# Performance work log

Hardware: AMD Instinct MI355X
Metric: run time of the kernel (lower is better)

Reference implementation:

```python
import jax, jax.numpy as jnp
import numpy as np

B, N, F_IN = 32, 512, 16
H, D_HID, D_OUT = 8, 8, 32
ALPHA = 0.2
NEG = -9e15


def setup_inputs() -> dict:
    key = jax.random.key(0)
    ks = jax.random.split(key, 10)
    xv = jax.random.normal(ks[0], (B, N, F_IN), dtype=jnp.float32)
    adj = (jax.random.uniform(ks[1], (B, N, N)) < 0.05).astype(jnp.float32)
    s = 0.1
    W_heads = jax.random.normal(ks[2], (H, F_IN, D_HID), dtype=jnp.float32) * s
    a1 = jax.random.normal(ks[3], (H, D_HID), dtype=jnp.float32) * s
    a2 = jax.random.normal(ks[4], (H, D_HID), dtype=jnp.float32) * s
    W_out = jax.random.normal(ks[5], (H * D_HID, D_OUT), dtype=jnp.float32) * s
    a1_out = jax.random.normal(ks[6], (D_OUT,), dtype=jnp.float32) * s
    a2_out = jax.random.normal(ks[7], (D_OUT,), dtype=jnp.float32) * s
    W_q = jax.random.normal(ks[8], (N * D_OUT, N), dtype=jnp.float32) * s
    b_q = jax.random.normal(ks[9], (N,), dtype=jnp.float32) * s
    return {"xv": xv, "adj": adj, "W_heads": W_heads, "a1": a1, "a2": a2,
            "W_out": W_out, "a1_out": a1_out, "a2_out": a2_out,
            "W_q": W_q, "b_q": b_q}


def _masked_softmax(e, adj_mask):
    # e: [..., N, N]; adj_mask broadcastable bool
    scores = jnp.where(adj_mask, e, NEG)
    return jax.nn.softmax(scores, axis=-1)


def reference(xv, adj, W_heads, a1, a2, W_out, a1_out, a2_out, W_q, b_q):
    mask = adj > 0  # [B, N, N]
    # --- multi-head GAT layer (vectorized over batch and heads) ---
    Wh = jnp.einsum('bnf,hfd->bhnd', xv, W_heads)            # [B,H,N,Dh]
    f1 = jnp.einsum('bhnd,hd->bhn', Wh, a1)                   # a^T[:Dh] . Wh_i
    f2 = jnp.einsum('bhnd,hd->bhn', Wh, a2)                   # a^T[Dh:] . Wh_j
    e = jax.nn.leaky_relu(f1[:, :, :, None] + f2[:, :, None, :], ALPHA)  # [B,H,N,N]
    att = _masked_softmax(e, mask[:, None, :, :])
    h = jnp.einsum('bhnm,bhmd->bhnd', att, Wh)
    h = jax.nn.elu(h)                                         # concat=True heads apply elu
    h_cat = jnp.transpose(h, (0, 2, 1, 3)).reshape(B, N, H * D_HID)  # head-major concat
    # --- output attention layer (concat=False: no internal elu) ---
    Who = jnp.einsum('bnf,fd->bnd', h_cat, W_out)             # [B,N,Do]
    g1 = Who @ a1_out                                         # [B,N]
    g2 = Who @ a2_out
    eo = jax.nn.leaky_relu(g1[:, :, None] + g2[:, None, :], ALPHA)
    att_o = _masked_softmax(eo, mask)
    out = jnp.einsum('bnm,bmd->bnd', att_o, Who)
    out = jax.nn.elu(out)                                     # F.elu applied in forward
    # --- Q head ---
    q = out.reshape(B, N * D_OUT) @ W_q + b_q                 # [B,N]
    return q[..., None]                                       # [B,N,1]
```

## Files before the change

### kernel.cpp

```cpp
#include <hip/hip_runtime.h>
#include <stdint.h>


typedef unsigned long long u64;

__device__ __forceinline__ float eluf(float x) { return x > 0.f ? x : __expf(x) - 1.f; }
__device__ __forceinline__ float lrelu(float x) { return fmaxf(x, 0.2f * x); }

__device__ u64   g_mask[131072];
__device__ float g_hcat[1048576];
__device__ float g_Who[524288];
__device__ float g_g1[16384];
__device__ float g_g2[16384];
__device__ float g_out2[524288];
__device__ float g_partial[4194304];

__global__ __launch_bounds__(256) void k_mask(const float* __restrict__ adj) {
  int wid = blockIdx.x * 4 + (threadIdx.x >> 6);
  int lane = threadIdx.x & 63;
#pragma unroll
  for (int seg = 0; seg < 16; ++seg) {
    int gw = wid * 16 + seg;
    float v = adj[(size_t)(gw >> 3) * 512 + (gw & 7) * 64 + lane];
    u64 bal = __ballot(v > 0.f);
    if (lane == 0) g_mask[gw] = bal;
  }
}

__global__ __launch_bounds__(512) void k_gat(const float* __restrict__ xv,
                                             const float* __restrict__ whd,
                                             const float* __restrict__ a1,
                                             const float* __restrict__ a2) {
  __shared__ float w_s[128];
  __shared__ float a1s[8], a2s[8];
  __shared__ float wh_lo[2048];
  __shared__ float wh_hi[2048];
  __shared__ float f2s[512];

  int bh = blockIdx.x;
  int b = bh >> 3, h = bh & 7;
  int tid = threadIdx.x;

  const u64* mrow = g_mask + (size_t)b * 4096 + (size_t)tid * 8;
  u64 mreg[8];
#pragma unroll
  for (int w = 0; w < 8; ++w) mreg[w] = mrow[w];

  if (tid < 128) w_s[tid] = whd[h * 128 + tid];
  if (tid < 8) { a1s[tid] = a1[h * 8 + tid]; a2s[tid] = a2[h * 8 + tid]; }
  __syncthreads();

  const float4* xp = (const float4*)(xv + (size_t)(b * 512 + tid) * 16);
  float x[16];
#pragma unroll
  for (int i = 0; i < 4; ++i) {
    float4 v = xp[i];
    x[4 * i] = v.x; x[4 * i + 1] = v.y; x[4 * i + 2] = v.z; x[4 * i + 3] = v.w;
  }
  float wh[8] = {0, 0, 0, 0, 0, 0, 0, 0};
#pragma unroll
  for (int f = 0; f < 16; ++f) {
    float xf = x[f];
#pragma unroll
    for (int d = 0; d < 8; ++d) wh[d] += xf * w_s[f * 8 + d];
  }
  float f1v = 0.f, s2 = 0.f;
#pragma unroll
  for (int d = 0; d < 8; ++d) { f1v += wh[d] * a1s[d]; s2 += wh[d] * a2s[d]; }
  f2s[tid] = s2;
  *(float4*)(wh_lo + tid * 4) = make_float4(wh[0], wh[1], wh[2], wh[3]);
  *(float4*)(wh_hi + tid * 4) = make_float4(wh[4], wh[5], wh[6], wh[7]);
  __syncthreads();

  float acc[8] = {0, 0, 0, 0, 0, 0, 0, 0};
  float sum = 0.f;
#pragma unroll
  for (int w = 0; w < 8; ++w) {
    u64 mq = mreg[w];
    while (mq) {
      int j = __builtin_ctzll(mq);
      mq &= mq - 1;
      int col = w * 64 + j;
      float p = __expf(lrelu(f1v + f2s[col]));
      sum += p;
      float4 A = *(const float4*)(wh_lo + col * 4);
      float4 Bv = *(const float4*)(wh_hi + col * 4);
      acc[0] += p * A.x;  acc[1] += p * A.y;  acc[2] += p * A.z;  acc[3] += p * A.w;
      acc[4] += p * Bv.x; acc[5] += p * Bv.y; acc[6] += p * Bv.z; acc[7] += p * Bv.w;
    }
  }

  float rs = sum > 0.f ? 1.0f / sum : 0.f;
  float* dst = g_hcat + (size_t)(b * 512 + tid) * 64 + h * 8;
  *(float4*)dst = make_float4(eluf(acc[0] * rs), eluf(acc[1] * rs), eluf(acc[2] * rs), eluf(acc[3] * rs));
  *(float4*)(dst + 4) = make_float4(eluf(acc[4] * rs), eluf(acc[5] * rs), eluf(acc[6] * rs), eluf(acc[7] * rs));
}

__global__ __launch_bounds__(128) void k_who(const float* __restrict__ wout,
                                             const float* __restrict__ a1o,
                                             const float* __restrict__ a2o) {
  __shared__ float wo_s[2048];
  __shared__ float a1s[32], a2s[32];
  int tid = threadIdx.x;
  for (int i = tid; i < 2048; i += 128) wo_s[i] = wout[i];
  if (tid < 32) { a1s[tid] = a1o[tid]; a2s[tid] = a2o[tid]; }
  __syncthreads();

  int idx = blockIdx.x * 128 + tid;
  int g = idx >> 1;
  int db = (idx & 1) * 16;

  const float4* hp = (const float4*)(g_hcat + (size_t)g * 64);
  float acc[16];
#pragma unroll
  for (int d = 0; d < 16; ++d) acc[d] = 0.f;
#pragma unroll
  for (int f4 = 0; f4 < 16; ++f4) {
    float4 h4 = hp[f4];
    float hv[4] = {h4.x, h4.y, h4.z, h4.w};
#pragma unroll
    for (int k = 0; k < 4; ++k) {
      const float* wr = wo_s + (f4 * 4 + k) * 32 + db;
      float hvk = hv[k];
#pragma unroll
      for (int d = 0; d < 16; ++d) acc[d] += hvk * wr[d];
    }
  }
  float s1 = 0.f, s2 = 0.f;
#pragma unroll
  for (int d = 0; d < 16; ++d) { s1 += acc[d] * a1s[db + d]; s2 += acc[d] * a2s[db + d]; }
  s1 += __shfl_xor(s1, 1);
  s2 += __shfl_xor(s2, 1);

  float* wdst = g_Who + (size_t)g * 32 + db;
#pragma unroll
  for (int d4 = 0; d4 < 4; ++d4)
    *(float4*)(wdst + d4 * 4) = make_float4(acc[d4 * 4], acc[d4 * 4 + 1], acc[d4 * 4 + 2], acc[d4 * 4 + 3]);
  if ((idx & 1) == 0) { g_g1[g] = s1; g_g2[g] = s2; }
}

__global__ __launch_bounds__(512) void k_att2() {
  __shared__ float pool[9216];
  __shared__ float g2c[256];
  __shared__ u64 mask_s[512];

  int b = blockIdx.x >> 3;
  int t = blockIdx.x & 7;
  int tid = threadIdx.x;
  int w = tid >> 6;
  int l = tid & 63;

  mask_s[tid] = g_mask[(size_t)b * 4096 + t * 512 + tid];
  float g1v = g_g1[(size_t)b * 512 + t * 64 + l];

  float acc[32];
#pragma unroll
  for (int d = 0; d < 32; ++d) acc[d] = 0.f;
  float sum = 0.f;

#pragma unroll 1
  for (int c = 0; c < 2; ++c) {
    __syncthreads();
    {
      const float4* src = (const float4*)g_Who + (size_t)b * 4096;
      for (int i = tid; i < 2048; i += 512) {
        int m = i >> 3, d4 = i & 7;
        *(float4*)(pool + m * 36 + d4 * 4) = src[c * 2048 + i];
      }
      if (tid < 64) ((float4*)g2c)[tid] = ((const float4*)g_g2)[(size_t)b * 128 + c * 64 + tid];
    }
    __syncthreads();
    u64 mq = mask_s[l * 8 + c * 4 + (w >> 1)];
    uint32_t bits = (w & 1) ? (uint32_t)(mq >> 32) : (uint32_t)mq;
    while (bits) {
      int j = __builtin_ctz(bits);
      bits &= bits - 1;
      float p = __expf(lrelu(g1v + g2c[w * 32 + j]));
      sum += p;
      const float* wq = pool + (w * 32 + j) * 36;
#pragma unroll
      for (int d4 = 0; d4 < 8; ++d4) {
        float4 v = *(const float4*)(wq + d4 * 4);
        acc[d4 * 4]     += p * v.x;
        acc[d4 * 4 + 1] += p * v.y;
        acc[d4 * 4 + 2] += p * v.z;
        acc[d4 * 4 + 3] += p * v.w;
      }
    }
  }

#pragma unroll 1
  for (int step = 4; step >= 1; step >>= 1) {
    __syncthreads();
    if (w >= step && w < 2 * step) {
      float* rp = pool + (size_t)((w - step) * 64 + l) * 36;
#pragma unroll
      for (int d4 = 0; d4 < 8; ++d4)
        *(float4*)(rp + d4 * 4) = make_float4(acc[d4 * 4], acc[d4 * 4 + 1], acc[d4 * 4 + 2], acc[d4 * 4 + 3]);
      rp[32] = sum;
    }
    __syncthreads();
    if (w < step) {
      const float* rp = pool + (size_t)(w * 64 + l) * 36;
#pragma unroll
      for (int d = 0; d < 32; ++d) acc[d] += rp[d];
      sum += rp[32];
    }
  }

  if (w == 0) {
    float rs = sum > 0.f ? 1.0f / sum : 0.f;
    float* dst = g_out2 + (size_t)(b * 512 + t * 64 + l) * 32;
#pragma unroll
    for (int d4 = 0; d4 < 8; ++d4)
      *(float4*)(dst + d4 * 4) = make_float4(eluf(acc[d4 * 4] * rs), eluf(acc[d4 * 4 + 1] * rs),
                                             eluf(acc[d4 * 4 + 2] * rs), eluf(acc[d4 * 4 + 3] * rs));
  }
}

__global__ __launch_bounds__(512) void k_qpart(const float* __restrict__ Wq) {
  __shared__ float outS[64 * 36];
  int s = blockIdx.x >> 1;
  int c = blockIdx.x & 1;
  int tid = threadIdx.x;
  int lane = tid & 63;
  int bg = tid >> 6;

  if (tid < 512) {
    int i = tid;
    int bb = i >> 4, kk4 = (i & 15) * 4;
    float4 v = *(const float4*)(g_out2 + (size_t)bb * 16384 + s * 64 + kk4);
    outS[(kk4 + 0) * 36 + bb] = v.x;
    outS[(kk4 + 1) * 36 + bb] = v.y;
    outS[(kk4 + 2) * 36 + bb] = v.z;
    outS[(kk4 + 3) * 36 + bb] = v.w;
  }
  __syncthreads();

  const float* wp = Wq + (size_t)(s * 64) * 512 + c * 256 + lane * 4;
  float4 acc[4];
#pragma unroll
  for (int j = 0; j < 4; ++j) acc[j] = make_float4(0.f, 0.f, 0.f, 0.f);

#pragma unroll 8
  for (int kk = 0; kk < 64; ++kk) {
    float4 wv = *(const float4*)(wp + (size_t)kk * 512);
    const float* ob = outS + kk * 36 + bg * 4;
    float4 o = *(const float4*)(ob);
    float ov[4] = {o.x, o.y, o.z, o.w};
#pragma unroll
    for (int j = 0; j < 4; ++j) {
      acc[j].x += ov[j] * wv.x; acc[j].y += ov[j] * wv.y;
      acc[j].z += ov[j] * wv.z; acc[j].w += ov[j] * wv.w;
    }
  }
#pragma unroll
  for (int j = 0; j < 4; ++j)
    *(float4*)(g_partial + (size_t)(s * 32 + bg * 4 + j) * 512 + c * 256 + lane * 4) = acc[j];
}

__global__ __launch_bounds__(256) void k_qred(const float* __restrict__ bq,
                                              float* __restrict__ out) {
  __shared__ float red[4][64];
  int tid = threadIdx.x;
  int w = tid >> 6, lane = tid & 63;
  int g = blockIdx.x * 64 + lane;
  int b = g >> 9, np = g & 511;

  float q = 0.f;
#pragma unroll 8
  for (int i = 0; i < 64; ++i) {
    int s = w + i * 4;
    q += g_partial[(size_t)(s * 32 + b) * 512 + np];
  }
  red[w][lane] = q;
  __syncthreads();
  if (w == 0)
    out[g] = bq[np] + red[0][lane] + red[1][lane] + red[2][lane] + red[3][lane];
}

extern "C" void kernel_launch(void* const* d_in, const int* in_sizes, int n_in,
                              void* d_out, int out_size, void* d_ws, size_t ws_size,
                              hipStream_t stream) {
  const float* xv = (const float*)d_in[0];
  const float* adj = (const float*)d_in[1];
  const float* W_heads = (const float*)d_in[2];
  const float* a1 = (const float*)d_in[3];
  const float* a2 = (const float*)d_in[4];
  const float* W_out = (const float*)d_in[5];
  const float* a1_out = (const float*)d_in[6];
  const float* a2_out = (const float*)d_in[7];
  const float* W_q = (const float*)d_in[8];
  const float* b_q = (const float*)d_in[9];

  k_mask<<<2048, 256, 0, stream>>>(adj);
  k_gat<<<256, 512, 0, stream>>>(xv, W_heads, a1, a2);
  k_who<<<256, 128, 0, stream>>>(W_out, a1_out, a2_out);
  k_att2<<<256, 512, 0, stream>>>();
  k_qpart<<<512, 512, 0, stream>>>(W_q);
  k_qred<<<256, 256, 0, stream>>>(b_q, (float*)d_out);
}
```

Baseline: 168.4 us.

## Fuse all six stages into one cooperative persistent kernel with grid syncs

Replaces the six separate kernel launches (mask, GAT heads, Who projection, output attention, Q partial GEMM, Q reduce) with a single cooperative kernel of 256 blocks separated by grid.sync barriers. Stage work is remapped to the fixed grid: the Q GEMM now covers 128 k-rows per block, halving the partial buffer and the reduction length, and the Who stage uses 8 threads per node. This removes per-launch overhead and inter-kernel gaps, at the cost of grid-wide barriers and fewer blocks in the mask and Q stages.

```diff
diff --git a/kernel.cpp b/kernel.cpp
--- a/kernel.cpp
+++ b/kernel.cpp
@@ -1,5 +1,8 @@
 #include <hip/hip_runtime.h>
+#include <hip/hip_cooperative_groups.h>
 #include <stdint.h>
+
+namespace cg = cooperative_groups;
 
 
 typedef unsigned long long u64;
@@ -7,276 +10,280 @@
 __device__ __forceinline__ float eluf(float x) { return x > 0.f ? x : __expf(x) - 1.f; }
 __device__ __forceinline__ float lrelu(float x) { return fmaxf(x, 0.2f * x); }
 
-__device__ u64   g_mask[131072];
-__device__ float g_hcat[1048576];
-__device__ float g_Who[524288];
-__device__ float g_g1[16384];
-__device__ float g_g2[16384];
-__device__ float g_out2[524288];
-__device__ float g_partial[4194304];
-
-__global__ __launch_bounds__(256) void k_mask(const float* __restrict__ adj) {
-  int wid = blockIdx.x * 4 + (threadIdx.x >> 6);
-  int lane = threadIdx.x & 63;
-#pragma unroll
-  for (int seg = 0; seg < 16; ++seg) {
-    int gw = wid * 16 + seg;
-    float v = adj[(size_t)(gw >> 3) * 512 + (gw & 7) * 64 + lane];
-    u64 bal = __ballot(v > 0.f);
-    if (lane == 0) g_mask[gw] = bal;
-  }
-}
-
-__global__ __launch_bounds__(512) void k_gat(const float* __restrict__ xv,
-                                             const float* __restrict__ whd,
-                                             const float* __restrict__ a1,
-                                             const float* __restrict__ a2) {
-  __shared__ float w_s[128];
-  __shared__ float a1s[8], a2s[8];
-  __shared__ float wh_lo[2048];
-  __shared__ float wh_hi[2048];
-  __shared__ float f2s[512];
-
-  int bh = blockIdx.x;
-  int b = bh >> 3, h = bh & 7;
-  int tid = threadIdx.x;
-
-  const u64* mrow = g_mask + (size_t)b * 4096 + (size_t)tid * 8;
-  u64 mreg[8];
-#pragma unroll
-  for (int w = 0; w < 8; ++w) mreg[w] = mrow[w];
-
-  if (tid < 128) w_s[tid] = whd[h * 128 + tid];
-  if (tid < 8) { a1s[tid] = a1[h * 8 + tid]; a2s[tid] = a2[h * 8 + tid]; }
-  __syncthreads();
-
-  const float4* xp = (const float4*)(xv + (size_t)(b * 512 + tid) * 16);
-  float x[16];
-#pragma unroll
-  for (int i = 0; i < 4; ++i) {
-    float4 v = xp[i];
-    x[4 * i] = v.x; x[4 * i + 1] = v.y; x[4 * i + 2] = v.z; x[4 * i + 3] = v.w;
-  }
-  float wh[8] = {0, 0, 0, 0, 0, 0, 0, 0};
-#pragma unroll
-  for (int f = 0; f < 16; ++f) {
-    float xf = x[f];
-#pragma unroll
-    for (int d = 0; d < 8; ++d) wh[d] += xf * w_s[f * 8 + d];
-  }
-  float f1v = 0.f, s2 = 0.f;
-#pragma unroll
-  for (int d = 0; d < 8; ++d) { f1v += wh[d] * a1s[d]; s2 += wh[d] * a2s[d]; }
-  f2s[tid] = s2;
-  *(float4*)(wh_lo + tid * 4) = make_float4(wh[0], wh[1], wh[2], wh[3]);
-  *(float4*)(wh_hi + tid * 4) = make_float4(wh[4], wh[5], wh[6], wh[7]);
-  __syncthreads();
-
-  float acc[8] = {0, 0, 0, 0, 0, 0, 0, 0};
-  float sum = 0.f;
-#pragma unroll
-  for (int w = 0; w < 8; ++w) {
-    u64 mq = mreg[w];
-    while (mq) {
-      int j = __builtin_ctzll(mq);
-      mq &= mq - 1;
-      int col = w * 64 + j;
-      float p = __expf(lrelu(f1v + f2s[col]));
-      sum += p;
-      float4 A = *(const float4*)(wh_lo + col * 4);
-      float4 Bv = *(const float4*)(wh_hi + col * 4);
-      acc[0] += p * A.x;  acc[1] += p * A.y;  acc[2] += p * A.z;  acc[3] += p * A.w;
-      acc[4] += p * Bv.x; acc[5] += p * Bv.y; acc[6] += p * Bv.z; acc[7] += p * Bv.w;
-    }
-  }
-
-  float rs = sum > 0.f ? 1.0f / sum : 0.f;
-  float* dst = g_hcat + (size_t)(b * 512 + tid) * 64 + h * 8;
-  *(float4*)dst = make_float4(eluf(acc[0] * rs), eluf(acc[1] * rs), eluf(acc[2] * rs), eluf(acc[3] * rs));
-  *(float4*)(dst + 4) = make_float4(eluf(acc[4] * rs), eluf(acc[5] * rs), eluf(acc[6] * rs), eluf(acc[7] * rs));
-}
-
-__global__ __launch_bounds__(128) void k_who(const float* __restrict__ wout,
-                                             const float* __restrict__ a1o,
-                                             const float* __restrict__ a2o) {
-  __shared__ float wo_s[2048];
-  __shared__ float a1s[32], a2s[32];
-  int tid = threadIdx.x;
-  for (int i = tid; i < 2048; i += 128) wo_s[i] = wout[i];
-  if (tid < 32) { a1s[tid] = a1o[tid]; a2s[tid] = a2o[tid]; }
-  __syncthreads();
-
-  int idx = blockIdx.x * 128 + tid;
-  int g = idx >> 1;
-  int db = (idx & 1) * 16;
-
-  const float4* hp = (const float4*)(g_hcat + (size_t)g * 64);
-  float acc[16];
-#pragma unroll
-  for (int d = 0; d < 16; ++d) acc[d] = 0.f;
-#pragma unroll
-  for (int f4 = 0; f4 < 16; ++f4) {
-    float4 h4 = hp[f4];
-    float hv[4] = {h4.x, h4.y, h4.z, h4.w};
-#pragma unroll
-    for (int k = 0; k < 4; ++k) {
-      const float* wr = wo_s + (f4 * 4 + k) * 32 + db;
-      float hvk = hv[k];
-#pragma unroll
-      for (int d = 0; d < 16; ++d) acc[d] += hvk * wr[d];
-    }
-  }
-  float s1 = 0.f, s2 = 0.f;
-#pragma unroll
-  for (int d = 0; d < 16; ++d) { s1 += acc[d] * a1s[db + d]; s2 += acc[d] * a2s[db + d]; }
-  s1 += __shfl_xor(s1, 1);
-  s2 += __shfl_xor(s2, 1);
-
-  float* wdst = g_Who + (size_t)g * 32 + db;
-#pragma unroll
-  for (int d4 = 0; d4 < 4; ++d4)
-    *(float4*)(wdst + d4 * 4) = make_float4(acc[d4 * 4], acc[d4 * 4 + 1], acc[d4 * 4 + 2], acc[d4 * 4 + 3]);
-  if ((idx & 1) == 0) { g_g1[g] = s1; g_g2[g] = s2; }
-}
-
-__global__ __launch_bounds__(512) void k_att2() {
-  __shared__ float pool[9216];
-  __shared__ float g2c[256];
-  __shared__ u64 mask_s[512];
-
-  int b = blockIdx.x >> 3;
-  int t = blockIdx.x & 7;
-  int tid = threadIdx.x;
-  int w = tid >> 6;
-  int l = tid & 63;
-
-  mask_s[tid] = g_mask[(size_t)b * 4096 + t * 512 + tid];
-  float g1v = g_g1[(size_t)b * 512 + t * 64 + l];
-
-  float acc[32];
-#pragma unroll
-  for (int d = 0; d < 32; ++d) acc[d] = 0.f;
-  float sum = 0.f;
-
+__device__ __align__(16) u64   g_mask[131072];
+__device__ __align__(16) float g_hcat[1048576];
+__device__ __align__(16) float g_Who[524288];
+__device__ __align__(16) float g_g1[16384];
+__device__ __align__(16) float g_g2[16384];
+__device__ __align__(16) float g_out2[524288];
+__device__ __align__(16) float g_partial[2097152];
+
+__global__ __launch_bounds__(512) void k_fused(
+    const float* __restrict__ xv, const float* __restrict__ adj,
+    const float* __restrict__ whd, const float* __restrict__ a1,
+    const float* __restrict__ a2, const float* __restrict__ wout,
+    const float* __restrict__ a1o, const float* __restrict__ a2o,
+    const float* __restrict__ Wq, const float* __restrict__ bq,
+    float* __restrict__ out) {
+  cg::grid_group grid = cg::this_grid();
+  __shared__ __align__(16) float smem[10496];
+  const int bid = blockIdx.x;
+  const int tid = threadIdx.x;
+  const int lane = tid & 63;
+  const int wvi = tid >> 6;
+
+  {
+    int r0 = (bid * 8 + wvi) * 8;
 #pragma unroll 1
-  for (int c = 0; c < 2; ++c) {
-    __syncthreads();
+    for (int rp = 0; rp < 4; ++rp) {
+      int row = r0 + rp * 2;
+      const float* ap = adj + (size_t)row * 512 + lane;
+      float v[16];
+#pragma unroll
+      for (int s = 0; s < 8; ++s) { v[s] = ap[s * 64]; v[8 + s] = ap[512 + s * 64]; }
+      u64* mp = g_mask + (size_t)row * 8;
+#pragma unroll
+      for (int s = 0; s < 8; ++s) {
+        u64 b0 = __ballot(v[s] > 0.f);
+        u64 b1 = __ballot(v[8 + s] > 0.f);
+        if (lane == 0) { mp[s] = b0; mp[8 + s] = b1; }
+      }
+    }
+  }
+  grid.sync();
+
+  {
+    float* w_s   = smem;
+    float* a1s   = smem + 128;
+    float* a2s   = smem + 136;
+    float* f2s   = smem + 144;
+    float* wh_lo = smem + 656;
+    float* wh_hi = smem + 2704;
+    int b = bid >> 3, h = bid & 7;
+    const u64* mrow = g_mask + (size_t)b * 4096 + (size_t)tid * 8;
+    u64 mreg[8];
+#pragma unroll
+    for (int w = 0; w < 8; ++w) mreg[w] = mrow[w];
+    if (tid < 128) w_s[tid] = whd[h * 128 + tid];
+    if (tid < 8) { a1s[tid] = a1[h * 8 + tid]; a2s[tid] = a2[h * 8 + tid]; }
+    __syncthreads();
+
+    const float4* xp = (const float4*)(xv + (size_t)(b * 512 + tid) * 16);
+    float x[16];
+#pragma unroll
+    for (int i = 0; i < 4; ++i) {
+      float4 v = xp[i];
+      x[4 * i] = v.x; x[4 * i + 1] = v.y; x[4 * i + 2] = v.z; x[4 * i + 3] = v.w;
+    }
+    float wh[8] = {0, 0, 0, 0, 0, 0, 0, 0};
+#pragma unroll
+    for (int f = 0; f < 16; ++f) {
+      float xf = x[f];
+#pragma unroll
+      for (int d = 0; d < 8; ++d) wh[d] += xf * w_s[f * 8 + d];
+    }
+    float f1v = 0.f, s2 = 0.f;
+#pragma unroll
+    for (int d = 0; d < 8; ++d) { f1v += wh[d] * a1s[d]; s2 += wh[d] * a2s[d]; }
+    f2s[tid] = s2;
+    *(float4*)(wh_lo + tid * 4) = make_float4(wh[0], wh[1], wh[2], wh[3]);
+    *(float4*)(wh_hi + tid * 4) = make_float4(wh[4], wh[5], wh[6], wh[7]);
+    __syncthreads();
+
+    float acc[8] = {0, 0, 0, 0, 0, 0, 0, 0};
+    float sum = 0.f;
+#pragma unroll
+    for (int w = 0; w < 8; ++w) {
+      u64 mq = mreg[w];
+      while (mq) {
+        int j = __builtin_ctzll(mq);
+        mq &= mq - 1;
+        int col = w * 64 + j;
+        float p = __expf(lrelu(f1v + f2s[col]));
+        sum += p;
+        float4 A = *(const float4*)(wh_lo + col * 4);
+        float4 Bv = *(const float4*)(wh_hi + col * 4);
+        acc[0] += p * A.x;  acc[1] += p * A.y;  acc[2] += p * A.z;  acc[3] += p * A.w;
+        acc[4] += p * Bv.x; acc[5] += p * Bv.y; acc[6] += p * Bv.z; acc[7] += p * Bv.w;
+      }
+    }
+    float rs = sum > 0.f ? 1.0f / sum : 0.f;
+    float* dst = g_hcat + (size_t)(b * 512 + tid) * 64 + h * 8;
+    *(float4*)dst = make_float4(eluf(acc[0] * rs), eluf(acc[1] * rs), eluf(acc[2] * rs), eluf(acc[3] * rs));
+    *(float4*)(dst + 4) = make_float4(eluf(acc[4] * rs), eluf(acc[5] * rs), eluf(acc[6] * rs), eluf(acc[7] * rs));
+  }
+  grid.sync();
+
+  {
+    float* wo_s = smem;
+    float* a1so = smem + 2048;
+    float* a2so = smem + 2080;
+    for (int i = tid; i < 2048; i += 512) wo_s[i] = wout[i];
+    if (tid < 32) { a1so[tid] = a1o[tid]; a2so[tid] = a2o[tid]; }
+    __syncthreads();
+
+    int gid = bid * 512 + tid;
+    int g = gid >> 3, sub = gid & 7, dq = sub * 4;
+    const float4* hp = (const float4*)(g_hcat + (size_t)g * 64);
+    float acc[4] = {0, 0, 0, 0};
+#pragma unroll
+    for (int f4 = 0; f4 < 16; ++f4) {
+      float4 h4 = hp[f4];
+      float hv[4] = {h4.x, h4.y, h4.z, h4.w};
+#pragma unroll
+      for (int k = 0; k < 4; ++k) {
+        float4 wv4 = *(const float4*)(wo_s + (f4 * 4 + k) * 32 + dq);
+        acc[0] += hv[k] * wv4.x; acc[1] += hv[k] * wv4.y;
+        acc[2] += hv[k] * wv4.z; acc[3] += hv[k] * wv4.w;
+      }
+    }
+    float s1 = acc[0] * a1so[dq] + acc[1] * a1so[dq + 1] + acc[2] * a1so[dq + 2] + acc[3] * a1so[dq + 3];
+    float s2 = acc[0] * a2so[dq] + acc[1] * a2so[dq + 1] + acc[2] * a2so[dq + 2] + acc[3] * a2so[dq + 3];
+    s1 += __shfl_xor(s1, 1); s1 += __shfl_xor(s1, 2); s1 += __shfl_xor(s1, 4);
+    s2 += __shfl_xor(s2, 1); s2 += __shfl_xor(s2, 2); s2 += __shfl_xor(s2, 4);
+    *(float4*)(g_Who + (size_t)g * 32 + dq) = make_float4(acc[0], acc[1], acc[2], acc[3]);
+    if (sub == 0) { g_g1[g] = s1; g_g2[g] = s2; }
+  }
+  grid.sync();
+
+  {
+    u64* mask_s = (u64*)smem;
+    float* pool = smem + 1024;
+    float* g2c  = smem + 10240;
+    int b = bid >> 3;
+    int t = bid & 7;
+    int w = wvi;
+    int l = lane;
+    mask_s[tid] = g_mask[(size_t)b * 4096 + t * 512 + tid];
+    float g1v = g_g1[(size_t)b * 512 + t * 64 + l];
+
+    float acc[32];
+#pragma unroll
+    for (int d = 0; d < 32; ++d) acc[d] = 0.f;
+    float sum = 0.f;
+
+#pragma unroll 1
+    for (int c = 0; c < 2; ++c) {
+      __syncthreads();
+      {
+        const float4* src = (const float4*)g_Who + (size_t)b * 4096;
+        for (int i = tid; i < 2048; i += 512) {
+          int m = i >> 3, d4 = i & 7;
+          *(float4*)(pool + m * 36 + d4 * 4) = src[c * 2048 + i];
+        }
+        if (tid < 64) ((float4*)g2c)[tid] = ((const float4*)g_g2)[(size_t)b * 128 + c * 64 + tid];
+      }
+      __syncthreads();
+      u64 mq = mask_s[l * 8 + c * 4 + (w >> 1)];
+      uint32_t bits = (w & 1) ? (uint32_t)(mq >> 32) : (uint32_t)mq;
+      while (bits) {
+        int j = __builtin_ctz(bits);
+        bits &= bits - 1;
+        float p = __expf(lrelu(g1v + g2c[w * 32 + j]));
+        sum += p;
+        const float* wq = pool + (w * 32 + j) * 36;
+#pragma unroll
+        for (int d4 = 0; d4 < 8; ++d4) {
+          float4 v = *(const float4*)(wq + d4 * 4);
+          acc[d4 * 4]     += p * v.x;
+          acc[d4 * 4 + 1] += p * v.y;
+          acc[d4 * 4 + 2] += p * v.z;
+          acc[d4 * 4 + 3] += p * v.w;
+        }
+      }
+    }
+
+#pragma unroll 1
+    for (int step = 4; step >= 1; step >>= 1) {
+      __syncthreads();
+      if (w >= step && w < 2 * step) {
+        float* rp = pool + (size_t)((w - step) * 64 + l) * 36;
+#pragma unroll
+        for (int d4 = 0; d4 < 8; ++d4)
+          *(float4*)(rp + d4 * 4) = make_float4(acc[d4 * 4], acc[d4 * 4 + 1], acc[d4 * 4 + 2], acc[d4 * 4 + 3]);
+        rp[32] = sum;
+      }
+      __syncthreads();
+      if (w < step) {
+        const float* rp = pool + (size_t)(w * 64 + l) * 36;
+#pragma unroll
+        for (int d = 0; d < 32; ++d) acc[d] += rp[d];
+        sum += rp[32];
+      }
+    }
+
+    if (w == 0) {
+      float rs = sum > 0.f ? 1.0f / sum : 0.f;
+      float* dst = g_out2 + (size_t)(b * 512 + t * 64 + l) * 32;
+#pragma unroll
+      for (int d4 = 0; d4 < 8; ++d4)
+        *(float4*)(dst + d4 * 4) = make_float4(eluf(acc[d4 * 4] * rs), eluf(acc[d4 * 4 + 1] * rs),
+                                               eluf(acc[d4 * 4 + 2] * rs), eluf(acc[d4 * 4 + 3] * rs));
+    }
+  }
+  grid.sync();
+
+  {
+    float* outS = smem;
+    int s = bid >> 1;
+    int c = bid & 1;
+    int bg = wvi;
     {
-      const float4* src = (const float4*)g_Who + (size_t)b * 4096;
-      for (int i = tid; i < 2048; i += 512) {
-        int m = i >> 3, d4 = i & 7;
-        *(float4*)(pool + m * 36 + d4 * 4) = src[c * 2048 + i];
-      }
-      if (tid < 64) ((float4*)g2c)[tid] = ((const float4*)g_g2)[(size_t)b * 128 + c * 64 + tid];
-    }
-    __syncthreads();
-    u64 mq = mask_s[l * 8 + c * 4 + (w >> 1)];
-    uint32_t bits = (w & 1) ? (uint32_t)(mq >> 32) : (uint32_t)mq;
-    while (bits) {
-      int j = __builtin_ctz(bits);
-      bits &= bits - 1;
-      float p = __expf(lrelu(g1v + g2c[w * 32 + j]));
-      sum += p;
-      const float* wq = pool + (w * 32 + j) * 36;
-#pragma unroll
-      for (int d4 = 0; d4 < 8; ++d4) {
-        float4 v = *(const float4*)(wq + d4 * 4);
-        acc[d4 * 4]     += p * v.x;
-        acc[d4 * 4 + 1] += p * v.y;
-        acc[d4 * 4 + 2] += p * v.z;
-        acc[d4 * 4 + 3] += p * v.w;
-      }
-    }
-  }
-
-#pragma unroll 1
-  for (int step = 4; step >= 1; step >>= 1) {
-    __syncthreads();
-    if (w >= step && w < 2 * step) {
-      float* rp = pool + (size_t)((w - step) * 64 + l) * 36;
-#pragma unroll
-      for (int d4 = 0; d4 < 8; ++d4)
-        *(float4*)(rp + d4 * 4) = make_float4(acc[d4 * 4], acc[d4 * 4 + 1], acc[d4 * 4 + 2], acc[d4 * 4 + 3]);
-      rp[32] = sum;
-    }
-    __syncthreads();
-    if (w < step) {
-      const float* rp = pool + (size_t)(w * 64 + l) * 36;
-#pragma unroll
-      for (int d = 0; d < 32; ++d) acc[d] += rp[d];
-      sum += rp[32];
-    }
-  }
-
-  if (w == 0) {
-    float rs = sum > 0.f ? 1.0f / sum : 0.f;
-    float* dst = g_out2 + (size_t)(b * 512 + t * 64 + l) * 32;
-#pragma unroll
-    for (int d4 = 0; d4 < 8; ++d4)
-      *(float4*)(dst + d4 * 4) = make_float4(eluf(acc[d4 * 4] * rs), eluf(acc[d4 * 4 + 1] * rs),
-                                             eluf(acc[d4 * 4 + 2] * rs), eluf(acc[d4 * 4 + 3] * rs));
-  }
-}
-
-__global__ __launch_bounds__(512) void k_qpart(const float* __restrict__ Wq) {
-  __shared__ float outS[64 * 36];
-  int s = blockIdx.x >> 1;
-  int c = blockIdx.x & 1;
-  int tid = threadIdx.x;
-  int lane = tid & 63;
-  int bg = tid >> 6;
-
-  if (tid < 512) {
-    int i = tid;
-    int bb = i >> 4, kk4 = (i & 15) * 4;
-    float4 v = *(const float4*)(g_out2 + (size_t)bb * 16384 + s * 64 + kk4);
-    outS[(kk4 + 0) * 36 + bb] = v.x;
-    outS[(kk4 + 1) * 36 + bb] = v.y;
-    outS[(kk4 + 2) * 36 + bb] = v.z;
-    outS[(kk4 + 3) * 36 + bb] = v.w;
-  }
-  __syncthreads();
-
-  const float* wp = Wq + (size_t)(s * 64) * 512 + c * 256 + lane * 4;
-  float4 acc[4];
-#pragma unroll
-  for (int j = 0; j < 4; ++j) acc[j] = make_float4(0.f, 0.f, 0.f, 0.f);
+      int bb = tid >> 4;
+      int kk8 = (tid & 15) * 8;
+      const float* src = g_out2 + (size_t)bb * 16384 + s * 128 + kk8;
+      float4 v0 = *(const float4*)src;
+      float4 v1 = *(const float4*)(src + 4);
+      outS[(kk8 + 0) * 36 + bb] = v0.x; outS[(kk8 + 1) * 36 + bb] = v0.y;
+      outS[(kk8 + 2) * 36 + bb] = v0.z; outS[(kk8 + 3) * 36 + bb] = v0.w;
+      outS[(kk8 + 4) * 36 + bb] = v1.x; outS[(kk8 + 5) * 36 + bb] = v1.y;
+      outS[(kk8 + 6) * 36 + bb] = v1.z; outS[(kk8 + 7) * 36 + bb] = v1.w;
+    }
+    __syncthreads();
+
+    const float* wp = Wq + (size_t)(s * 128) * 512 + c * 256 + lane * 4;
+    float4 acc4[4];
+#pragma unroll
+    for (int j = 0; j < 4; ++j) acc4[j] = make_float4(0.f, 0.f, 0.f, 0.f);
 
 #pragma unroll 8
-  for (int kk = 0; kk < 64; ++kk) {
-    float4 wv = *(const float4*)(wp + (size_t)kk * 512);
-    const float* ob = outS + kk * 36 + bg * 4;
-    float4 o = *(const float4*)(ob);
-    float ov[4] = {o.x, o.y, o.z, o.w};
-#pragma unroll
-    for (int j = 0; j < 4; ++j) {
-      acc[j].x += ov[j] * wv.x; acc[j].y += ov[j] * wv.y;
-      acc[j].z += ov[j] * wv.z; acc[j].w += ov[j] * wv.w;
-    }
-  }
-#pragma unroll
-  for (int j = 0; j < 4; ++j)
-    *(float4*)(g_partial + (size_t)(s * 32 + bg * 4 + j) * 512 + c * 256 + lane * 4) = acc[j];
-}
-
-__global__ __launch_bounds__(256) void k_qred(const float* __restrict__ bq,
-                                              float* __restrict__ out) {
-  __shared__ float red[4][64];
-  int tid = threadIdx.x;
-  int w = tid >> 6, lane = tid & 63;
-  int g = blockIdx.x * 64 + lane;
-  int b = g >> 9, np = g & 511;
-
-  float q = 0.f;
-#pragma unroll 8
-  for (int i = 0; i < 64; ++i) {
-    int s = w + i * 4;
-    q += g_partial[(size_t)(s * 32 + b) * 512 + np];
-  }
-  red[w][lane] = q;
-  __syncthreads();
-  if (w == 0)
-    out[g] = bq[np] + red[0][lane] + red[1][lane] + red[2][lane] + red[3][lane];
+    for (int kk = 0; kk < 128; ++kk) {
+      float4 wv4 = *(const float4*)(wp + (size_t)kk * 512);
+      const float* ob = outS + kk * 36 + bg * 4;
+      float4 o = *(const float4*)ob;
+      float ov[4] = {o.x, o.y, o.z, o.w};
+#pragma unroll
+      for (int j = 0; j < 4; ++j) {
+        acc4[j].x += ov[j] * wv4.x; acc4[j].y += ov[j] * wv4.y;
+        acc4[j].z += ov[j] * wv4.z; acc4[j].w += ov[j] * wv4.w;
+      }
+    }
+#pragma unroll
+    for (int j = 0; j < 4; ++j)
+      *(float4*)(g_partial + (size_t)(s * 32 + bg * 4 + j) * 512 + c * 256 + lane * 4) = acc4[j];
+  }
+  grid.sync();
+
+  {
+    float* red = smem;
+    int w = wvi, l = lane;
+    int g = bid * 64 + l;
+    int b = g >> 9, np = g & 511;
+    float q = 0.f;
+#pragma unroll
+    for (int i = 0; i < 16; ++i) {
+      int s = w + i * 8;
+      q += g_partial[(size_t)(s * 32 + b) * 512 + np];
+    }
+    red[w * 64 + l] = q;
+    __syncthreads();
+    if (w == 0) {
+      float tacc = bq[np];
+#pragma unroll
+      for (int k = 0; k < 8; ++k) tacc += red[k * 64 + l];
+      out[g] = tacc;
+    }
+  }
 }
 
 extern "C" void kernel_launch(void* const* d_in, const int* in_sizes, int n_in,
@@ -292,11 +299,11 @@
   const float* a2_out = (const float*)d_in[7];
   const float* W_q = (const float*)d_in[8];
   const float* b_q = (const float*)d_in[9];
-
-  k_mask<<<2048, 256, 0, stream>>>(adj);
-  k_gat<<<256, 512, 0, stream>>>(xv, W_heads, a1, a2);
-  k_who<<<256, 128, 0, stream>>>(W_out, a1_out, a2_out);
-  k_att2<<<256, 512, 0, stream>>>();
-  k_qpart<<<512, 512, 0, stream>>>(W_q);
-  k_qred<<<256, 256, 0, stream>>>(b_q, (float*)d_out);
+  float* outp = (float*)d_out;
+
+  void* args[] = {(void*)&xv, (void*)&adj, (void*)&W_heads, (void*)&a1, (void*)&a2,
+                  (void*)&W_out, (void*)&a1_out, (void*)&a2_out, (void*)&W_q,
+                  (void*)&b_q, (void*)&outp};
+  hipLaunchCooperativeKernel(reinterpret_cast<void*>(k_fused), dim3(256), dim3(512),
+                             args, 0, stream);
 }
```

Measured after the change: 336.4 us. 99.8% more time.
